# Kernel optimization log

Hardware: AMD Instinct MI355X
Metric: run time of the kernel (lower is better)

The kernel has to match this reference:

```python
import jax, jax.numpy as jnp
import numpy as np

N_NODES = 100000
E2 = 1600000
E3 = 1600000
ES = 100000
HID = 64


def _mlp_3x3(x_in, W1, b1, W2, b2):
    # x_in: [E, d_in] -> mobility [E, 3, 3]
    h = jax.nn.relu(x_in @ W1 + b1)
    out = h @ W2 + b2  # [E, 9]
    return out.reshape(-1, 3, 3)


def setup_inputs() -> dict:
    key = jax.random.key(0)
    ks = jax.random.split(key, 20)
    inp = {}
    inp["x"] = jax.random.normal(ks[0], (N_NODES, 3), dtype=jnp.float32)
    inp["edge_2body"] = jax.random.randint(ks[1], (2, E2), 0, N_NODES)
    inp["edge_3body"] = jax.random.randint(ks[2], (3, E3), 0, N_NODES)
    inp["edge_2bodySelf"] = jax.random.randint(ks[3], (2, ES), 0, N_NODES)
    inp["edge_1body"] = jax.random.randint(ks[4], (2, ES), 0, N_NODES)
    inp["edge_attr_2body"] = jax.random.normal(ks[5], (E2, 3), dtype=jnp.float32)
    inp["edge_attr_3body"] = jax.random.normal(ks[6], (E3, 3), dtype=jnp.float32)
    inp["edge_attr_2bodySelf"] = jax.random.normal(ks[7], (ES, 3), dtype=jnp.float32)
    inp["edge_attr_1body"] = jax.random.normal(ks[8], (ES, 3), dtype=jnp.float32)
    s = 0.1
    # nn_2body: 3 -> HID -> 9
    inp["W1_2b"] = jax.random.normal(ks[9], (3, HID), dtype=jnp.float32) * s
    inp["b1_2b"] = jnp.zeros((HID,), jnp.float32)
    inp["W2_2b"] = jax.random.normal(ks[10], (HID, 9), dtype=jnp.float32) * s
    inp["b2_2b"] = jnp.zeros((9,), jnp.float32)
    # nn_3body: 6 -> HID -> 9
    inp["W1_3b"] = jax.random.normal(ks[11], (6, HID), dtype=jnp.float32) * s
    inp["b1_3b"] = jnp.zeros((HID,), jnp.float32)
    inp["W2_3b"] = jax.random.normal(ks[12], (HID, 9), dtype=jnp.float32) * s
    inp["b2_3b"] = jnp.zeros((9,), jnp.float32)
    # nn_self: 3 -> HID -> 9
    inp["W1_s"] = jax.random.normal(ks[13], (3, HID), dtype=jnp.float32) * s
    inp["b1_s"] = jnp.zeros((HID,), jnp.float32)
    inp["W2_s"] = jax.random.normal(ks[14], (HID, 9), dtype=jnp.float32) * s
    inp["b2_s"] = jnp.zeros((9,), jnp.float32)
    return inp


def reference(x, edge_2body, edge_3body, edge_2bodySelf, edge_1body,
              edge_attr_2body, edge_attr_3body, edge_attr_2bodySelf, edge_attr_1body,
              W1_2b, b1_2b, W2_2b, b2_2b,
              W1_3b, b1_3b, W2_3b, b2_3b,
              W1_s, b1_s, W2_s, b2_s):
    n = x.shape[0]
    # ---- 2-body: gather -> MLP -> per-edge 3x3 matvec -> scatter-add ----
    d2 = x[edge_2body[0]] - x[edge_2body[1]]  # xj - xi, [E2,3]
    mob2 = _mlp_3x3(d2, W1_2b, b1_2b, W2_2b, b2_2b)
    y2 = jnp.einsum('eij,ej->ei', mob2, edge_attr_2body)
    v2 = jax.ops.segment_sum(y2, edge_2body[1], num_segments=n)
    # ---- 3-body ----
    xj = x[edge_3body[0]]
    xk = x[edge_3body[1]]
    xi = x[edge_3body[2]]
    d3 = jnp.concatenate((xk - xj, xi - xk), axis=1)  # [E3,6]
    mob3 = _mlp_3x3(d3, W1_3b, b1_3b, W2_3b, b2_3b)
    y3 = jnp.einsum('eij,ej->ei', mob3, edge_attr_3body)
    v3 = jax.ops.segment_sum(y3, edge_3body[2], num_segments=n)
    # ---- 2-body self ----
    ds = x[edge_2bodySelf[0]] - x[edge_2bodySelf[1]]
    mobs = _mlp_3x3(ds, W1_s, b1_s, W2_s, b2_s)
    ys = jnp.einsum('eij,ej->ei', mobs, edge_attr_2bodySelf)
    vs = jax.ops.segment_sum(ys, edge_2bodySelf[1], num_segments=n)
    # edge_1body / edge_attr_1body unused in original forward
    return v2 + v3 + vs
```

## Files before the change

kernel.cpp:

```cpp
#include <hip/hip_runtime.h>


constexpr int HIDDEN = 64;
constexpr int NB_MAX = 256;
constexpr int NPB_SHIFT = 9;
constexpr int NPB = 1 << NPB_SHIFT;
constexpr int TILE_F = NPB * 3;
constexpr int NET_SLOT = 1040;
constexpr int PSPLIT = 4;

typedef _Float16 h2_t __attribute__((ext_vector_type(2)));

__device__ __forceinline__ unsigned packh2(float a, float b) {
    auto h = __builtin_amdgcn_cvt_pkrtz(a, b);
    return __builtin_bit_cast(unsigned, h);
}
__device__ __forceinline__ float fdot2u(unsigned a, unsigned b, float c) {
    h2_t ha = __builtin_bit_cast(h2_t, a);
    h2_t hb = __builtin_bit_cast(h2_t, b);
#if __has_builtin(__builtin_amdgcn_fdot2)
    return __builtin_amdgcn_fdot2(ha, hb, c, false);
#else
    return fmaf((float)ha.x, (float)hb.x, fmaf((float)ha.y, (float)hb.y, c));
#endif
}


__global__ __launch_bounds__(256) void setup_kernel(
    const float* __restrict__ x, int n_nodes, float4* __restrict__ x4,
    int* __restrict__ gcount, float* __restrict__ out,
    const float* __restrict__ W1_2b, const float* __restrict__ b1_2b,
    const float* __restrict__ W2_2b, const float* __restrict__ b2_2b,
    const float* __restrict__ W1_s,  const float* __restrict__ b1_s,
    const float* __restrict__ W2_s,  const float* __restrict__ b2_s,
    const float* __restrict__ W1_3b, const float* __restrict__ b1_3b,
    const float* __restrict__ W2_3b, const float* __restrict__ b2_3b,
    unsigned* __restrict__ nets)
{
    const int blk = blockIdx.x;
    const int tid = threadIdx.x;
    if (blk < 3) {
        const float *W1, *b1, *W2, *b2; int din;
        if (blk == 0) { W1 = W1_2b; b1 = b1_2b; W2 = W2_2b; b2 = b2_2b; din = 3; }
        else if (blk == 1) { W1 = W1_s; b1 = b1_s; W2 = W2_s; b2 = b2_s; din = 3; }
        else { W1 = W1_3b; b1 = b1_3b; W2 = W2_3b; b2 = b2_3b; din = 6; }
        unsigned* slot = nets + blk * NET_SLOT;
        float* slotf = (float*)slot;
        if (tid < 32) {
            const int h2 = tid, hA = 2 * h2, hB = 2 * h2 + 1;
            if (din == 3) {
                unsigned* row = slot + h2 * 16;
                float* rowf = (float*)row;
                row[0] = packh2(W1[0 * HIDDEN + hA], W1[1 * HIDDEN + hA]);
                row[1] = packh2(W1[0 * HIDDEN + hB], W1[1 * HIDDEN + hB]);
                rowf[2] = b1[hA]; rowf[3] = b1[hB];
                rowf[4] = W1[2 * HIDDEN + hA]; rowf[5] = W1[2 * HIDDEN + hB];
                #pragma unroll
                for (int i = 0; i < 9; ++i)
                    row[6 + i] = packh2(W2[hA * 9 + i], W2[hB * 9 + i]);
                row[15] = 0;
            } else {
                unsigned* row = slot + h2 * 32;
                float* rowf = (float*)row;
                #pragma unroll
                for (int r = 0; r < 3; ++r) {
                    row[r]     = packh2(W1[(2 * r) * HIDDEN + hA], W1[(2 * r + 1) * HIDDEN + hA]);
                    row[3 + r] = packh2(W1[(2 * r) * HIDDEN + hB], W1[(2 * r + 1) * HIDDEN + hB]);
                }
                rowf[6] = b1[hA]; rowf[7] = b1[hB];
                #pragma unroll
                for (int i = 0; i < 9; ++i)
                    row[8 + i] = packh2(W2[hA * 9 + i], W2[hB * 9 + i]);
                #pragma unroll
                for (int i = 17; i < 20; ++i) row[i] = 0;
            }
        }
        if (tid >= 32 && tid < 41) slotf[1024 + (tid - 32)] = b2[tid - 32];
        if (blk == 0) gcount[tid] = 0;
    } else {
        int i = (blk - 3) * 256 + tid;
        if (i < n_nodes) {
            x4[i] = make_float4(x[3 * i], x[3 * i + 1], x[3 * i + 2], 0.0f);
            out[3 * i + 0] = 0.0f;
            out[3 * i + 1] = 0.0f;
            out[3 * i + 2] = 0.0f;
        }
    }
}

__global__ __launch_bounds__(256) void p1_edge_kernel(
    const float4* __restrict__ x4,
    const int* __restrict__ e0, long long E0, const float* __restrict__ at0,
    const int* __restrict__ e1, long long E1, const float* __restrict__ at1,
    const int* __restrict__ e2, long long E2, const float* __restrict__ at2,
    int g0, int g1,
    const unsigned* __restrict__ nets,
    float4* __restrict__ records, int* __restrict__ gcount, int cap)
{
    constexpr int BLK = 256;
    constexpr int KPT = 4;
    static_assert(NB_MAX == BLK, "one reserve bin per thread");

    __shared__ int s_hist[NB_MAX];
    __shared__ int s_base[NB_MAX];
    __shared__ int s_rank[NB_MAX];
    __shared__ __align__(16) unsigned s_net[1033];

    const int gA = g0 + g1;
    const int gB = (int)gridDim.x - gA;
    const int mn = (gA < gB) ? gA : gB;
    int aidx = -1, b6 = -1;
    {
        const int idx = blockIdx.x;
        if (idx < 2 * mn) { if (idx & 1) b6 = idx >> 1; else aidx = idx >> 1; }
        else {
            const int r = idx - 2 * mn;
            if (gA > gB) aidx = mn + r; else b6 = mn + r;
        }
    }

    const int* edges; long long E; const float* attr;
    int bidx, nblk, din3;
    const unsigned* wp;
    if (aidx >= 0) {
        if (aidx < g0) { edges = e0; E = E0; attr = at0; bidx = aidx;      nblk = g0; din3 = 1; wp = nets; }
        else           { edges = e1; E = E1; attr = at1; bidx = aidx - g0; nblk = g1; din3 = 1; wp = nets + NET_SLOT; }
    } else             { edges = e2; E = E2; attr = at2; bidx = b6;        nblk = gB; din3 = 0; wp = nets + 2 * NET_SLOT; }

    const int tid = threadIdx.x;
    long long span = (E + nblk - 1) / nblk;
    span = (span + 1023) & ~1023LL;
    const long long lo = (long long)bidx * span;
    const long long hi = (lo + span < E) ? (lo + span) : E;
    if (lo >= E) return;

    const bool e_aligned = ((E & 3) == 0);

    for (int i = tid; i < NB_MAX; i += BLK) { s_hist[i] = 0; s_rank[i] = 0; }
    const int nstage = din3 ? 512 : 1024;
    for (int i = tid; i < nstage; i += BLK) s_net[i] = wp[i];
    if (tid < 9) s_net[1024 + tid] = wp[1024 + tid];
    __syncthreads();

    const unsigned* w = s_net;
    const float* wf = (const float*)s_net;

    float b2r[9];
    #pragma unroll
    for (int i = 0; i < 9; ++i) b2r[i] = wf[1024 + i];

    const long long dstrow = din3 ? E : 2 * E;
    for (long long t0 = lo; t0 < hi; t0 += BLK * KPT) {
        const long long be = t0 + (long long)tid * KPT;
        if (be >= hi) continue;
        if (e_aligned && be + KPT <= hi) {
            int4 r = *(const int4*)(edges + dstrow + be);
            atomicAdd(&s_hist[r.x >> NPB_SHIFT], 1);
            atomicAdd(&s_hist[r.y >> NPB_SHIFT], 1);
            atomicAdd(&s_hist[r.z >> NPB_SHIFT], 1);
            atomicAdd(&s_hist[r.w >> NPB_SHIFT], 1);
        } else {
            #pragma unroll
            for (int u = 0; u < KPT; ++u) {
                long long e = be + u;
                if (e < hi)
                    atomicAdd(&s_hist[edges[dstrow + e] >> NPB_SHIFT], 1);
            }
        }
    }
    __syncthreads();

    int my_base = 0;
    {
        const int h = s_hist[tid];
        if (h > 0) my_base = atomicAdd(&gcount[tid], h);
    }

    bool first = true;
    for (long long t0 = lo; t0 < hi; t0 += BLK * KPT) {
        const long long be = t0 + (long long)tid * KPT;

        unsigned dp[KPT][3];
        float    d2s[KPT];
        float    a[KPT][3];
        int      dst[KPT];
        bool     valid[KPT];
        int      i0[KPT], i1[KPT], i2[KPT];

        const bool full = e_aligned && (be + KPT <= hi);
        if (full) {
            int4 r0 = *(const int4*)(edges + be);
            int4 r1 = *(const int4*)(edges + E + be);
            i0[0] = r0.x; i0[1] = r0.y; i0[2] = r0.z; i0[3] = r0.w;
            i1[0] = r1.x; i1[1] = r1.y; i1[2] = r1.z; i1[3] = r1.w;
            if (!din3) {
                int4 r2 = *(const int4*)(edges + 2 * E + be);
                i2[0] = r2.x; i2[1] = r2.y; i2[2] = r2.z; i2[3] = r2.w;
            }
            float4 a0 = *(const float4*)(attr + 3 * be);
            float4 a1 = *(const float4*)(attr + 3 * be + 4);
            float4 a2 = *(const float4*)(attr + 3 * be + 8);
            a[0][0] = a0.x; a[0][1] = a0.y; a[0][2] = a0.z;
            a[1][0] = a0.w; a[1][1] = a1.x; a[1][2] = a1.y;
            a[2][0] = a1.z; a[2][1] = a1.w; a[2][2] = a2.x;
            a[3][0] = a2.y; a[3][1] = a2.z; a[3][2] = a2.w;
            #pragma unroll
            for (int u = 0; u < KPT; ++u) valid[u] = true;
        } else {
            #pragma unroll
            for (int u = 0; u < KPT; ++u) {
                long long e = be + u;
                valid[u] = (e < hi);
                long long ee = valid[u] ? e : lo;
                i0[u] = edges[ee];
                i1[u] = edges[E + ee];
                if (!din3) i2[u] = edges[2 * E + ee];
                #pragma unroll
                for (int c = 0; c < 3; ++c) a[u][c] = attr[3 * ee + c];
            }
        }

        #pragma unroll
        for (int u = 0; u < KPT; ++u) {
            if (din3) {
                dst[u] = i1[u];
                float4 xs = x4[i0[u]];
                float4 xt = x4[i1[u]];
                dp[u][0] = packh2(xs.x - xt.x, xs.y - xt.y);
                d2s[u]   = xs.z - xt.z;
                dp[u][1] = 0; dp[u][2] = 0;
            } else {
                dst[u] = i2[u];
                float4 xj = x4[i0[u]];
                float4 xk = x4[i1[u]];
                float4 xi = x4[i2[u]];
                dp[u][0] = packh2(xk.x - xj.x, xk.y - xj.y);
                dp[u][1] = packh2(xk.z - xj.z, xi.x - xk.x);
                dp[u][2] = packh2(xi.y - xk.y, xi.z - xk.z);
                d2s[u] = 0.f;
            }
        }

        float acc[KPT][9];
        #pragma unroll
        for (int u = 0; u < KPT; ++u)
            #pragma unroll
            for (int i = 0; i < 9; ++i) acc[u][i] = b2r[i];

        if (din3) {
            #pragma unroll 2
            for (int hh2 = 0; hh2 < HIDDEN / 2; ++hh2) {
                const uint4* rq = (const uint4*)(w + (hh2 << 4));
                const uint4 q0 = rq[0], q1 = rq[1], q2 = rq[2], q3 = rq[3];
                const unsigned wA = q0.x;
                const unsigned wB = q0.y;
                const float bbA = __uint_as_float(q0.z);
                const float bbB = __uint_as_float(q0.w);
                const float wcA = __uint_as_float(q1.x);
                const float wcB = __uint_as_float(q1.y);
                const unsigned w2p[9] = {q1.z, q1.w, q2.x, q2.y, q2.z,
                                         q2.w, q3.x, q3.y, q3.z};
                #pragma unroll
                for (int u = 0; u < KPT; ++u) {
                    float preA = fmaf(d2s[u], wcA, fdot2u(dp[u][0], wA, bbA));
                    float preB = fmaf(d2s[u], wcB, fdot2u(dp[u][0], wB, bbB));
                    unsigned h2 = packh2(fmaxf(preA, 0.f), fmaxf(preB, 0.f));
                    #pragma unroll
                    for (int i = 0; i < 9; ++i)
                        acc[u][i] = fdot2u(h2, w2p[i], acc[u][i]);
                }
            }
        } else {
            #pragma unroll 2
            for (int hh2 = 0; hh2 < HIDDEN / 2; ++hh2) {
                const uint4* rq = (const uint4*)(w + (hh2 << 5));
                const uint4 q0 = rq[0], q1 = rq[1], q2 = rq[2], q3 = rq[3];
                const unsigned q4x = w[(hh2 << 5) + 16];
                const unsigned wA0 = q0.x, wA1 = q0.y, wA2 = q0.z;
                const unsigned wB0 = q0.w, wB1 = q1.x, wB2 = q1.y;
                const float bbA = __uint_as_float(q1.z);
                const float bbB = __uint_as_float(q1.w);
                const unsigned w2p[9] = {q2.x, q2.y, q2.z, q2.w, q3.x,
                                         q3.y, q3.z, q3.w, q4x};
                #pragma unroll
                for (int u = 0; u < KPT; ++u) {
                    float preA = fdot2u(dp[u][2], wA2,
                                 fdot2u(dp[u][1], wA1,
                                 fdot2u(dp[u][0], wA0, bbA)));
                    float preB = fdot2u(dp[u][2], wB2,
                                 fdot2u(dp[u][1], wB1,
                                 fdot2u(dp[u][0], wB0, bbB)));
                    unsigned h2 = packh2(fmaxf(preA, 0.f), fmaxf(preB, 0.f));
                    #pragma unroll
                    for (int i = 0; i < 9; ++i)
                        acc[u][i] = fdot2u(h2, w2p[i], acc[u][i]);
                }
            }
        }

        if (first) {
            s_base[tid] = my_base;
            __syncthreads();
            first = false;
        }

        #pragma unroll
        for (int u = 0; u < KPT; ++u) {
            if (!valid[u]) continue;
            float y0 = fmaf(acc[u][0], a[u][0], fmaf(acc[u][1], a[u][1], acc[u][2] * a[u][2]));
            float y1 = fmaf(acc[u][3], a[u][0], fmaf(acc[u][4], a[u][1], acc[u][5] * a[u][2]));
            float y2 = fmaf(acc[u][6], a[u][0], fmaf(acc[u][7], a[u][1], acc[u][8] * a[u][2]));
            int b = dst[u] >> NPB_SHIFT;
            int r = atomicAdd(&s_rank[b], 1);
            int slot = s_base[b] + r;
            if (slot < cap)
                records[(size_t)b * cap + slot] =
                    make_float4(y0, y1, y2, __int_as_float(dst[u]));
        }
    }
}

__global__ __launch_bounds__(512) void p2_bucket(
    const float4* __restrict__ records, const int* __restrict__ gcount,
    int cap, int n_nodes, float* __restrict__ out)
{
    __shared__ float s_acc[TILE_F];
    const int b = blockIdx.x / PSPLIT;
    const int part = blockIdx.x % PSPLIT;
    const int tid = threadIdx.x;

    for (int i = tid; i < TILE_F; i += 512) s_acc[i] = 0.0f;
    __syncthreads();

    int cnt = gcount[b];
    if (cnt > cap) cnt = cap;
    const float4* rb = records + (size_t)b * cap;
    for (int i = part * 512 + tid; i < cnt; i += 512 * PSPLIT) {
        float4 r = rb[i];
        int loc = __float_as_int(r.w) - (b << NPB_SHIFT);
        atomicAdd(&s_acc[loc * 3 + 0], r.x);
        atomicAdd(&s_acc[loc * 3 + 1], r.y);
        atomicAdd(&s_acc[loc * 3 + 2], r.z);
    }
    __syncthreads();

    const int start = (b << NPB_SHIFT) * 3;
    const int end = min(n_nodes * 3, ((b + 1) << NPB_SHIFT) * 3);
    for (int i = start + tid; i < end; i += 512) {
        float v = s_acc[i - start];
        if (v != 0.0f) atomicAdd(&out[i], v);
    }
}

template <int DIN, int KPT>
__global__ __launch_bounds__(256) void edge_mlp_atomic(
    const float* __restrict__ x,
    const int* __restrict__ edges, long long E,
    const float* __restrict__ attr,
    const float* __restrict__ W1, const float* __restrict__ b1,
    const float* __restrict__ W2, const float* __restrict__ b2,
    float* __restrict__ out)
{
    const int tid = threadIdx.x;
    const long long base = (long long)blockIdx.x * (blockDim.x * KPT) + tid;
    float d[KPT][DIN]; float a[KPT][3]; int dst[KPT]; bool valid[KPT];
    #pragma unroll
    for (int u = 0; u < KPT; ++u) {
        long long e = base + (long long)u * blockDim.x;
        valid[u] = (e < E);
        long long ee = valid[u] ? e : 0;
        if constexpr (DIN == 3) {
            int s = edges[ee]; int t = edges[E + ee]; dst[u] = t;
            #pragma unroll
            for (int c = 0; c < 3; ++c)
                d[u][c] = x[3 * (long long)s + c] - x[3 * (long long)t + c];
        } else {
            int j = edges[ee]; int k = edges[E + ee]; int i = edges[2 * E + ee];
            dst[u] = i;
            #pragma unroll
            for (int c = 0; c < 3; ++c) {
                float xj = x[3 * (long long)j + c];
                float xk = x[3 * (long long)k + c];
                float xi = x[3 * (long long)i + c];
                d[u][c] = xk - xj; d[u][3 + c] = xi - xk;
            }
        }
        #pragma unroll
        for (int c = 0; c < 3; ++c) a[u][c] = attr[3 * ee + c];
    }
    float acc[KPT][9];
    #pragma unroll
    for (int u = 0; u < KPT; ++u)
        #pragma unroll
        for (int i = 0; i < 9; ++i) acc[u][i] = b2[i];
    #pragma unroll 4
    for (int hh = 0; hh < HIDDEN; ++hh) {
        const float bb = b1[hh];
        float w1r[DIN];
        #pragma unroll
        for (int r = 0; r < DIN; ++r) w1r[r] = W1[r * HIDDEN + hh];
        float w2r[9];
        #pragma unroll
        for (int i = 0; i < 9; ++i) w2r[i] = W2[hh * 9 + i];
        #pragma unroll
        for (int u = 0; u < KPT; ++u) {
            float pre = bb;
            #pragma unroll
            for (int r = 0; r < DIN; ++r) pre = fmaf(d[u][r], w1r[r], pre);
            const float h = fmaxf(pre, 0.0f);
            #pragma unroll
            for (int i = 0; i < 9; ++i) acc[u][i] = fmaf(h, w2r[i], acc[u][i]);
        }
    }
    #pragma unroll
    for (int u = 0; u < KPT; ++u) {
        if (!valid[u]) continue;
        float* o = out + 3 * (long long)dst[u];
        #pragma unroll
        for (int i = 0; i < 3; ++i) {
            float y = fmaf(acc[u][3 * i + 0], a[u][0],
                      fmaf(acc[u][3 * i + 1], a[u][1],
                           acc[u][3 * i + 2] * a[u][2]));
            atomicAdd(&o[i], y);
        }
    }
}

extern "C" void kernel_launch(void* const* d_in, const int* in_sizes, int n_in,
                              void* d_out, int out_size, void* d_ws, size_t ws_size,
                              hipStream_t stream)
{
    const float* x  = (const float*)d_in[0];
    const int*   e2 = (const int*)d_in[1];
    const int*   e3 = (const int*)d_in[2];
    const int*   es = (const int*)d_in[3];
    const float* a2 = (const float*)d_in[5];
    const float* a3 = (const float*)d_in[6];
    const float* as = (const float*)d_in[7];
    const float* W1_2b = (const float*)d_in[9];
    const float* b1_2b = (const float*)d_in[10];
    const float* W2_2b = (const float*)d_in[11];
    const float* b2_2b = (const float*)d_in[12];
    const float* W1_3b = (const float*)d_in[13];
    const float* b1_3b = (const float*)d_in[14];
    const float* W2_3b = (const float*)d_in[15];
    const float* b2_3b = (const float*)d_in[16];
    const float* W1_s  = (const float*)d_in[17];
    const float* b1_s  = (const float*)d_in[18];
    const float* W2_s  = (const float*)d_in[19];
    const float* b2_s  = (const float*)d_in[20];

    const long long E2 = in_sizes[1] / 2;
    const long long E3 = in_sizes[2] / 3;
    const long long ES = in_sizes[3] / 2;
    const long long Etot = E2 + E3 + ES;
    const int n_nodes = out_size / 3;
    const int nbuckets = (n_nodes + NPB - 1) >> NPB_SHIFT;

    float* out = (float*)d_out;

    const size_t off_nets = 1024;
    const size_t off_x4 = off_nets + 3 * NET_SLOT * 4;
    const size_t x4_bytes = (size_t)n_nodes * sizeof(float4);
    const size_t off_rec = (off_x4 + x4_bytes + 255) & ~(size_t)255;

    long long mean_per_bucket = (Etot + nbuckets - 1) / nbuckets;
    long long min_cap = mean_per_bucket + 1600;
    long long cap_avail =
        ((long long)ws_size - (long long)off_rec) / ((long long)nbuckets * 16);

    constexpr int SPAN = 1024;
    int g0 = (int)((E2 + SPAN - 1) / SPAN);
    int g1 = (int)((ES + SPAN - 1) / SPAN);
    int g2g = (int)((E3 + SPAN - 1) / SPAN);

    if (nbuckets <= NB_MAX && cap_avail >= min_cap) {
        long long capL = min_cap + 4096;
        if (capL > cap_avail) capL = cap_avail;
        int cap = (int)capL;
        int* gcount = (int*)d_ws;
        unsigned* nets = (unsigned*)((char*)d_ws + off_nets);
        float4* x4 = (float4*)((char*)d_ws + off_x4);
        float4* records = (float4*)((char*)d_ws + off_rec);

        int nb_pad = (n_nodes + 255) / 256;
        setup_kernel<<<3 + nb_pad, 256, 0, stream>>>(
            x, n_nodes, x4, gcount, out,
            W1_2b, b1_2b, W2_2b, b2_2b,
            W1_s,  b1_s,  W2_s,  b2_s,
            W1_3b, b1_3b, W2_3b, b2_3b,
            nets);

        p1_edge_kernel<<<g0 + g1 + g2g, 256, 0, stream>>>(
            x4,
            e2, E2, a2,
            es, ES, as,
            e3, E3, a3,
            g0, g1,
            nets, records, gcount, cap);

        p2_bucket<<<nbuckets * PSPLIT, 512, 0, stream>>>(records, gcount, cap, n_nodes, out);
    } else {
        hipMemsetAsync(out, 0, (size_t)out_size * sizeof(float), stream);
        constexpr int BLK = 256, KPT = 4;
        const long long per_blk = (long long)BLK * KPT;
        int a2g = (int)((E2 + per_blk - 1) / per_blk);
        int a3g = (int)((E3 + per_blk - 1) / per_blk);
        int asg = (int)((ES + per_blk - 1) / per_blk);
        if (a2g > 0)
            edge_mlp_atomic<3, KPT><<<a2g, BLK, 0, stream>>>(
                x, e2, E2, a2, W1_2b, b1_2b, W2_2b, b2_2b, out);
        if (a3g > 0)
            edge_mlp_atomic<6, KPT><<<a3g, BLK, 0, stream>>>(
                x, e3, E3, a3, W1_3b, b1_3b, W2_3b, b2_3b, out);
        if (asg > 0)
            edge_mlp_atomic<3, KPT><<<asg, BLK, 0, stream>>>(
                x, es, ES, as, W1_s, b1_s, W2_s, b2_s, out);
    }
}
```

Measured before the change: 313.0 us.

## Replace bucketed record scatter with direct global atomic accumulation

Drops the two-phase scheme, which histogrammed destinations into buckets, wrote per-edge float4 records and reduced them per bucket in shared memory. Each edge now adds its 3-vector straight into the output with global float atomics. This removes the histogram pass, the record write and read-back, and the second kernel launch. The cost is about 3.3M edges times 3 scattered global atomics onto 100k nodes, which may contend or serialize in L2.

```diff
diff --git a/kernel.cpp b/kernel.cpp
--- a/kernel.cpp
+++ b/kernel.cpp
@@ -2,12 +2,7 @@
 
 
 constexpr int HIDDEN = 64;
-constexpr int NB_MAX = 256;
-constexpr int NPB_SHIFT = 9;
-constexpr int NPB = 1 << NPB_SHIFT;
-constexpr int TILE_F = NPB * 3;
 constexpr int NET_SLOT = 1040;
-constexpr int PSPLIT = 4;
 
 typedef _Float16 h2_t __attribute__((ext_vector_type(2)));
 
@@ -28,7 +23,7 @@
 
 __global__ __launch_bounds__(256) void setup_kernel(
     const float* __restrict__ x, int n_nodes, float4* __restrict__ x4,
-    int* __restrict__ gcount, float* __restrict__ out,
+    float* __restrict__ out,
     const float* __restrict__ W1_2b, const float* __restrict__ b1_2b,
     const float* __restrict__ W2_2b, const float* __restrict__ b2_2b,
     const float* __restrict__ W1_s,  const float* __restrict__ b1_s,
@@ -76,7 +71,6 @@
             }
         }
         if (tid >= 32 && tid < 41) slotf[1024 + (tid - 32)] = b2[tid - 32];
-        if (blk == 0) gcount[tid] = 0;
     } else {
         int i = (blk - 3) * 256 + tid;
         if (i < n_nodes) {
@@ -88,22 +82,18 @@
     }
 }
 
-__global__ __launch_bounds__(256) void p1_edge_kernel(
+__global__ __launch_bounds__(256) void p1_direct_kernel(
     const float4* __restrict__ x4,
     const int* __restrict__ e0, long long E0, const float* __restrict__ at0,
     const int* __restrict__ e1, long long E1, const float* __restrict__ at1,
     const int* __restrict__ e2, long long E2, const float* __restrict__ at2,
     int g0, int g1,
     const unsigned* __restrict__ nets,
-    float4* __restrict__ records, int* __restrict__ gcount, int cap)
+    float* __restrict__ out)
 {
     constexpr int BLK = 256;
     constexpr int KPT = 4;
-    static_assert(NB_MAX == BLK, "one reserve bin per thread");
-
-    __shared__ int s_hist[NB_MAX];
-    __shared__ int s_base[NB_MAX];
-    __shared__ int s_rank[NB_MAX];
+
     __shared__ __align__(16) unsigned s_net[1033];
 
     const int gA = g0 + g1;
@@ -136,7 +126,6 @@
 
     const bool e_aligned = ((E & 3) == 0);
 
-    for (int i = tid; i < NB_MAX; i += BLK) { s_hist[i] = 0; s_rank[i] = 0; }
     const int nstage = din3 ? 512 : 1024;
     for (int i = tid; i < nstage; i += BLK) s_net[i] = wp[i];
     if (tid < 9) s_net[1024 + tid] = wp[1024 + tid];
@@ -149,34 +138,6 @@
     #pragma unroll
     for (int i = 0; i < 9; ++i) b2r[i] = wf[1024 + i];
 
-    const long long dstrow = din3 ? E : 2 * E;
-    for (long long t0 = lo; t0 < hi; t0 += BLK * KPT) {
-        const long long be = t0 + (long long)tid * KPT;
-        if (be >= hi) continue;
-        if (e_aligned && be + KPT <= hi) {
-            int4 r = *(const int4*)(edges + dstrow + be);
-            atomicAdd(&s_hist[r.x >> NPB_SHIFT], 1);
-            atomicAdd(&s_hist[r.y >> NPB_SHIFT], 1);
-            atomicAdd(&s_hist[r.z >> NPB_SHIFT], 1);
-            atomicAdd(&s_hist[r.w >> NPB_SHIFT], 1);
-        } else {
-            #pragma unroll
-            for (int u = 0; u < KPT; ++u) {
-                long long e = be + u;
-                if (e < hi)
-                    atomicAdd(&s_hist[edges[dstrow + e] >> NPB_SHIFT], 1);
-            }
-        }
-    }
-    __syncthreads();
-
-    int my_base = 0;
-    {
-        const int h = s_hist[tid];
-        if (h > 0) my_base = atomicAdd(&gcount[tid], h);
-    }
-
-    bool first = true;
     for (long long t0 = lo; t0 < hi; t0 += BLK * KPT) {
         const long long be = t0 + (long long)tid * KPT;
 
@@ -186,6 +147,8 @@
         int      dst[KPT];
         bool     valid[KPT];
         int      i0[KPT], i1[KPT], i2[KPT];
+
+        if (be >= hi) continue;
 
         const bool full = e_aligned && (be + KPT <= hi);
         if (full) {
@@ -298,57 +261,17 @@
             }
         }
 
-        if (first) {
-            s_base[tid] = my_base;
-            __syncthreads();
-            first = false;
-        }
-
         #pragma unroll
         for (int u = 0; u < KPT; ++u) {
             if (!valid[u]) continue;
             float y0 = fmaf(acc[u][0], a[u][0], fmaf(acc[u][1], a[u][1], acc[u][2] * a[u][2]));
             float y1 = fmaf(acc[u][3], a[u][0], fmaf(acc[u][4], a[u][1], acc[u][5] * a[u][2]));
             float y2 = fmaf(acc[u][6], a[u][0], fmaf(acc[u][7], a[u][1], acc[u][8] * a[u][2]));
-            int b = dst[u] >> NPB_SHIFT;
-            int r = atomicAdd(&s_rank[b], 1);
-            int slot = s_base[b] + r;
-            if (slot < cap)
-                records[(size_t)b * cap + slot] =
-                    make_float4(y0, y1, y2, __int_as_float(dst[u]));
-        }
-    }
-}
-
-__global__ __launch_bounds__(512) void p2_bucket(
-    const float4* __restrict__ records, const int* __restrict__ gcount,
-    int cap, int n_nodes, float* __restrict__ out)
-{
-    __shared__ float s_acc[TILE_F];
-    const int b = blockIdx.x / PSPLIT;
-    const int part = blockIdx.x % PSPLIT;
-    const int tid = threadIdx.x;
-
-    for (int i = tid; i < TILE_F; i += 512) s_acc[i] = 0.0f;
-    __syncthreads();
-
-    int cnt = gcount[b];
-    if (cnt > cap) cnt = cap;
-    const float4* rb = records + (size_t)b * cap;
-    for (int i = part * 512 + tid; i < cnt; i += 512 * PSPLIT) {
-        float4 r = rb[i];
-        int loc = __float_as_int(r.w) - (b << NPB_SHIFT);
-        atomicAdd(&s_acc[loc * 3 + 0], r.x);
-        atomicAdd(&s_acc[loc * 3 + 1], r.y);
-        atomicAdd(&s_acc[loc * 3 + 2], r.z);
-    }
-    __syncthreads();
-
-    const int start = (b << NPB_SHIFT) * 3;
-    const int end = min(n_nodes * 3, ((b + 1) << NPB_SHIFT) * 3);
-    for (int i = start + tid; i < end; i += 512) {
-        float v = s_acc[i - start];
-        if (v != 0.0f) atomicAdd(&out[i], v);
+            float* o = out + 3 * (long long)dst[u];
+            atomicAdd(&o[0], y0);
+            atomicAdd(&o[1], y1);
+            atomicAdd(&o[2], y2);
+        }
     }
 }
 
@@ -453,53 +376,38 @@
     const long long E2 = in_sizes[1] / 2;
     const long long E3 = in_sizes[2] / 3;
     const long long ES = in_sizes[3] / 2;
-    const long long Etot = E2 + E3 + ES;
     const int n_nodes = out_size / 3;
-    const int nbuckets = (n_nodes + NPB - 1) >> NPB_SHIFT;
 
     float* out = (float*)d_out;
 
-    const size_t off_nets = 1024;
-    const size_t off_x4 = off_nets + 3 * NET_SLOT * 4;
+    const size_t off_x4 = ((3 * NET_SLOT * 4) + 255) & ~(size_t)255;
     const size_t x4_bytes = (size_t)n_nodes * sizeof(float4);
-    const size_t off_rec = (off_x4 + x4_bytes + 255) & ~(size_t)255;
-
-    long long mean_per_bucket = (Etot + nbuckets - 1) / nbuckets;
-    long long min_cap = mean_per_bucket + 1600;
-    long long cap_avail =
-        ((long long)ws_size - (long long)off_rec) / ((long long)nbuckets * 16);
+    const size_t ws_need = off_x4 + x4_bytes;
 
     constexpr int SPAN = 1024;
     int g0 = (int)((E2 + SPAN - 1) / SPAN);
     int g1 = (int)((ES + SPAN - 1) / SPAN);
     int g2g = (int)((E3 + SPAN - 1) / SPAN);
 
-    if (nbuckets <= NB_MAX && cap_avail >= min_cap) {
-        long long capL = min_cap + 4096;
-        if (capL > cap_avail) capL = cap_avail;
-        int cap = (int)capL;
-        int* gcount = (int*)d_ws;
-        unsigned* nets = (unsigned*)((char*)d_ws + off_nets);
+    if (ws_size >= ws_need) {
+        unsigned* nets = (unsigned*)d_ws;
         float4* x4 = (float4*)((char*)d_ws + off_x4);
-        float4* records = (float4*)((char*)d_ws + off_rec);
 
         int nb_pad = (n_nodes + 255) / 256;
         setup_kernel<<<3 + nb_pad, 256, 0, stream>>>(
-            x, n_nodes, x4, gcount, out,
+            x, n_nodes, x4, out,
             W1_2b, b1_2b, W2_2b, b2_2b,
             W1_s,  b1_s,  W2_s,  b2_s,
             W1_3b, b1_3b, W2_3b, b2_3b,
             nets);
 
-        p1_edge_kernel<<<g0 + g1 + g2g, 256, 0, stream>>>(
+        p1_direct_kernel<<<g0 + g1 + g2g, 256, 0, stream>>>(
             x4,
             e2, E2, a2,
             es, ES, as,
             e3, E3, a3,
             g0, g1,
-            nets, records, gcount, cap);
-
-        p2_bucket<<<nbuckets * PSPLIT, 512, 0, stream>>>(records, gcount, cap, n_nodes, out);
+            nets, out);
     } else {
         hipMemsetAsync(out, 0, (size_t)out_size * sizeof(float), stream);
         constexpr int BLK = 256, KPT = 4;
```

Result: slower. 629.2 us (+101.0%).
